# Performance work log

Hardware: AMD Instinct MI355X
Metric: run time of the kernel (lower is better)

Reference implementation:

```python
import jax, jax.numpy as jnp
import numpy as np
from jax import lax

B, D, H, W = 4, 32, 256, 256
ALPHA = 4.0     # init arg alpha
KFRAMES = 4.0   # self.K = alpha
EPS_BN = 1e-5

def FT2d(a):
    return jnp.fft.fft2(a, axes=(-2, -1))

def iFT2d(a):
    return jnp.fft.ifft2(a, axes=(-2, -1))

def forward_proj(field, otf):
    # field [B,D,H,W] real, otf [B,D,H,W] complex -> min-max scaled |holo| [B,1,H,W]
    Fholo = jnp.sum(FT2d(field.astype(jnp.complex64)) * otf, axis=1, keepdims=True)
    holo = jnp.abs(iFT2d(Fholo))
    mn = holo.min(axis=(-2, -1), keepdims=True)
    mx = holo.max(axis=(-2, -1), keepdims=True)
    return (holo - mn) / (mx - mn)

def back_proj(holo, otf):
    # holo [B,1,H,W] real -> real field [B,D,H,W]; broadcasting over depth == tile+FFT
    Fh = FT2d(holo.astype(jnp.complex64))
    return jnp.real(iFT2d(Fh * jnp.conj(otf)))

def cbl(xin, w, g, b, act):
    y = lax.conv_general_dilated(xin, w, (1, 1), 'SAME',
                                 dimension_numbers=('NCHW', 'OIHW', 'NCHW'))
    m = y.mean(axis=(0, 2, 3), keepdims=True)
    v = y.var(axis=(0, 2, 3), keepdims=True)  # biased var, torch BN training-mode
    y = (y - m) * lax.rsqrt(v + EPS_BN) * g[None, :, None, None] + b[None, :, None, None]
    return jax.nn.leaky_relu(y, 0.01) if act else y

def resblock(xin, wa, ga, ba, wb, gb, bb):
    h = cbl(cbl(xin, wa, ga, ba, True), wb, gb, bb, False)
    return jax.nn.leaky_relu(xin + h, 0.01)

def plholonet_forward(phi, z, u1, u2, otf, K1f, rho1, rho2, soft_thr, p):
    # ---- X update: FFT-domain proximal solve ----
    x1 = phi - u1
    x2 = z - u2
    n = rho1 * back_proj(x1, otf) + rho2 * x2
    d = (rho2 + jnp.abs(otf) ** 2 * rho1).astype(jnp.complex64)
    x = jnp.real(iFT2d(FT2d(n.astype(jnp.complex64)) / d))
    # ---- Phi update: vectorized 30-step masked bisection ----
    phi_tilde = forward_proj(x, otf) + u1
    K0 = 1.0 - K1f
    c = ALPHA / KFRAMES
    def func(y):
        return c * (K0 - K1f / (jnp.exp(c * y) - 1.0)) + rho1 * (y - phi_tilde)
    ind0_init = K1f == 0
    phimin = jnp.full_like(phi_tilde, 1e-5)
    phimax = jnp.full_like(phi_tilde, 100.0)
    phiave = 0.5 * (phimin + phimax)
    def step(carry, _):
        pmin, pmax, pave, ind0 = carry
        ind1 = jnp.logical_not(ind0)
        t = func(pave)
        pmin = jnp.where((t > 0) & ind1, pave, pmin)
        pmax = jnp.where((t < 0) & ind1, pave, pmax)
        ind0 = ind0 | ((t == 0) & ind1)
        pave = jnp.where(jnp.logical_not(ind0), 0.5 * (pmin + pmax), pave)
        return (pmin, pmax, pave, ind0), None
    (_, _, phiave, _), _ = lax.scan(step, (phimin, phimax, phiave, ind0_init), None, length=30)
    phi_next = jnp.where(ind0_init, phi_tilde - K0 / rho1, phiave)
    # ---- Z update: denoiser with symmetry loss ----
    z_tilde = x + u2
    h1 = resblock(z_tilde, p['w1a'], p['g1a'], p['b1a'], p['w1b'], p['g1b'], p['b1b'])
    h1_thr = jnp.sign(h1) * jax.nn.relu(jnp.abs(h1) - soft_thr)
    z_next = resblock(h1_thr, p['w2a'], p['g2a'], p['b2a'], p['w2b'], p['g2b'], p['b2b'])
    x_fb = resblock(h1, p['w2a'], p['g2a'], p['b2a'], p['w2b'], p['g2b'], p['b2b'])
    stage_symloss = x_fb - z_tilde
    # ---- dual updates ----
    u1_next = u1 + phi_next - forward_proj(x, otf)
    u2_next = u2 + z_next - x
    return (x, phi_next, z_next, u1_next, u2_next, stage_symloss)

def setup_inputs() -> dict:
    key = jax.random.key(0)
    ks = jax.random.split(key, 16)
    f = jnp.float32
    inp = dict(
        x=jax.random.normal(ks[0], (B, D, H, W), f),
        phi=jax.random.uniform(ks[1], (B, 1, H, W), dtype=f),
        z=jax.random.normal(ks[2], (B, D, H, W), f) * 0.1,
        u1=jax.random.uniform(ks[3], (B, 1, H, W), dtype=f) * 0.1,
        u2=jax.random.uniform(ks[4], (B, D, H, W), dtype=f) * 0.1,
        otf_real=jax.random.normal(ks[5], (B, D, H, W), f) * 0.5,
        otf_imag=jax.random.normal(ks[6], (B, D, H, W), f) * 0.5,
        K1=jax.random.randint(ks[7], (B, 1, H, W), 0, 5, jnp.int32),
        rho1=jnp.array([0.7], f),
        rho2=jnp.array([0.5], f),
        soft_thr=jnp.array([0.01], f),
    )
    for i, sfx in enumerate(['1a', '1b', '2a', '2b']):
        inp['w' + sfx] = jax.random.normal(ks[8 + i], (D, D, 3, 3), f) * 0.05
        inp['g' + sfx] = jnp.ones((D,), f)
        inp['b' + sfx] = jnp.zeros((D,), f)
    return inp

def reference(x, phi, z, u1, u2, otf_real, otf_imag, K1, rho1, rho2, soft_thr,
              w1a, g1a, b1a, w1b, g1b, b1b, w2a, g2a, b2a, w2b, g2b, b2b):
    # note: the torch forward immediately overwrites its `x` argument via X_update,
    # so the input x is unused (kept in the signature for interface faithfulness).
    otf = (otf_real + 1j * otf_imag).astype(jnp.complex64)
    K1f = K1.astype(jnp.float32)
    p = dict(w1a=w1a, g1a=g1a, b1a=b1a, w1b=w1b, g1b=g1b, b1b=b1b,
             w2a=w2a, g2a=g2a, b2a=b2a, w2b=w2b, g2b=g2b, b2b=b2b)
    return plholonet_forward(phi, z, u1, u2, otf, K1f, rho1, rho2, soft_thr, p)
```

## Files before the change

kernel.cpp:

```cpp
#include <hip/hip_runtime.h>
#include <math.h>

#define WDIM 256
#define HW   65536

struct cplx { float x, y; };
__device__ __forceinline__ cplx cmul(cplx a, cplx b){ return {a.x*b.x - a.y*b.y, a.x*b.y + a.y*b.x}; }
__device__ __forceinline__ cplx cadd(cplx a, cplx b){ return {a.x+b.x, a.y+b.y}; }
__device__ __forceinline__ cplx csub(cplx a, cplx b){ return {a.x-b.x, a.y-b.y}; }
__device__ __forceinline__ void swapc(cplx& a, cplx& b){ cplx t=a; a=b; b=t; }

typedef __attribute__((ext_vector_type(8))) short short8;
typedef __attribute__((ext_vector_type(4))) float float4v;

__device__ __forceinline__ unsigned short f2bf(float f){
  unsigned int u = __float_as_uint(f);
  unsigned int r = (u + 0x7FFFu + ((u >> 16) & 1u)) >> 16;
  return (unsigned short)r;
}
__device__ __forceinline__ float bf2f(unsigned short h){
  return __uint_as_float(((unsigned int)h) << 16);
}

template<bool INV>
__device__ __forceinline__ void fft16(cplx v[16]) {
  const float C16[8] = {1.f, 0.9238795325112867f, 0.7071067811865476f, 0.3826834323650898f,
                        0.f, -0.3826834323650898f, -0.7071067811865476f, -0.9238795325112867f};
  const float S16[8] = {0.f, 0.3826834323650898f, 0.7071067811865476f, 0.9238795325112867f,
                        1.f, 0.9238795325112867f, 0.7071067811865476f, 0.3826834323650898f};
  swapc(v[1], v[8]); swapc(v[2], v[4]); swapc(v[3], v[12]);
  swapc(v[5], v[10]); swapc(v[7], v[14]); swapc(v[11], v[13]);
  #pragma unroll
  for (int s = 1; s <= 4; ++s) {
    const int m = 1 << s, half = m >> 1, step = 16 >> s;
    #pragma unroll
    for (int k = 0; k < 16; k += m) {
      #pragma unroll
      for (int j = 0; j < half; ++j) {
        cplx w = {C16[j*step], INV ? S16[j*step] : -S16[j*step]};
        cplx t = cmul(w, v[k+j+half]);
        v[k+j+half] = csub(v[k+j], t);
        v[k+j]      = cadd(v[k+j], t);
      }
    }
  }
}

template<bool INV>
__device__ void fft256_16(cplx v[16], int t, cplx* Yu) {
  fft16<INV>(v);
  float ang = (INV ? 6.283185307179586f : -6.283185307179586f) * (float)t * (1.0f/256.0f);
  float sn, cs; sincosf(ang, &sn, &cs);
  cplx wstep = {cs, sn}, w = {1.f, 0.f};
  #pragma unroll
  for (int c = 0; c < 16; ++c) { v[c] = cmul(v[c], w); w = cmul(w, wstep); }
  __syncthreads();
  #pragma unroll
  for (int c = 0; c < 16; ++c) Yu[t*17 + c] = v[c];
  __syncthreads();
  cplx z[16];
  #pragma unroll
  for (int b = 0; b < 16; ++b) z[b] = Yu[b*17 + t];
  fft16<INV>(z);
  #pragma unroll
  for (int d = 0; d < 16; ++d) v[d] = z[d];
  __syncthreads();
}

__global__ __launch_bounds__(256) void k_row_fwd_all(const float* __restrict__ a,
                                                     const float* __restrict__ b,
                                                     const float* __restrict__ sa,
                                                     const float* __restrict__ sb,
                                                     cplx* __restrict__ P,
                                                     cplx* __restrict__ XS) {
  __shared__ cplx Y[16*280];
  int unit = threadIdx.x >> 4, t = threadIdx.x & 15;
  int bp = blockIdx.y;
  size_t rowoff = (size_t)(blockIdx.x*16 + unit)*WDIM;
  const float *pa, *pb;
  size_t base0, baseo_rel;
  cplx* outb;
  if (bp < 64) {
    int bb = bp >> 4, p = bp & 15;
    pa = a; pb = b;
    base0 = ((size_t)(bb*32 + 2*p))*HW + rowoff;
    outb = P; baseo_rel = (size_t)bp*HW + rowoff;
  } else {
    int pp = bp - 64;
    pa = sa; pb = sb;
    base0 = ((size_t)(2*pp))*HW + rowoff;
    outb = XS; baseo_rel = (size_t)pp*HW + rowoff;
  }
  size_t base1 = base0 + HW;
  cplx v[16];
  #pragma unroll
  for (int i = 0; i < 16; ++i) {
    size_t o = i*16 + t;
    v[i] = {pa[base0+o] - pb[base0+o], pa[base1+o] - pb[base1+o]};
  }
  fft256_16<false>(v, t, Y + unit*280);
  #pragma unroll
  for (int d = 0; d < 16; ++d) outb[baseo_rel + t + 16*d] = v[d];
}

template<bool INV>
__device__ void col_core(const cplx* __restrict__ in, cplx* lds, cplx v[16], size_t planeBase) {
  int tid = threadIdx.x;
  #pragma unroll
  for (int i = 0; i < 16; ++i) {
    int idx = tid + 256*i; int h = idx >> 4, w = idx & 15;
    lds[h*17 + w] = in[planeBase + (size_t)h*WDIM + w];
  }
  __syncthreads();
  int u = tid >> 4, t = tid & 15;
  cplx vv[16];
  #pragma unroll
  for (int a = 0; a < 16; ++a) vv[a] = lds[(16*a + t)*17 + u];
  fft256_16<INV>(vv, t, lds + u*280);
  #pragma unroll
  for (int d = 0; d < 16; ++d) v[d] = vv[d];
}

__global__ __launch_bounds__(256) void k_col_fwd_all(cplx* __restrict__ P,
                                                     cplx* __restrict__ XS) {
  __shared__ cplx lds[4480];
  int y = blockIdx.y;
  cplx* buf = (y < 64) ? (P + (size_t)y*HW) : (XS + (size_t)(y-64)*HW);
  size_t planeBase = blockIdx.x*16;
  cplx v[16];
  col_core<false>(buf, lds, v, planeBase);
  int u = threadIdx.x >> 4, t = threadIdx.x & 15;
  #pragma unroll
  for (int d = 0; d < 16; ++d) lds[(t + 16*d)*17 + u] = v[d];
  __syncthreads();
  int tid = threadIdx.x;
  #pragma unroll
  for (int i = 0; i < 16; ++i) {
    int idx = tid + 256*i; int h = idx >> 4, w = idx & 15;
    buf[planeBase + (size_t)h*WDIM + w] = lds[h*17 + w];
  }
}

__global__ __launch_bounds__(256) void k_row_inv_all(const cplx* __restrict__ Q,
                                                     const cplx* __restrict__ HFT,
                                                     cplx* __restrict__ W2,
                                                     cplx* __restrict__ XS) {
  __shared__ cplx Y[16*280];
  int unit = threadIdx.x >> 4, t = threadIdx.x & 15;
  int y = blockIdx.y;
  const cplx* inb;  cplx* outb;
  if (y < 64) { inb = Q + (size_t)y*HW; outb = W2 + (size_t)y*HW; }
  else        { inb = HFT + (size_t)(y-64)*HW; outb = XS + (size_t)(y-64)*HW; }
  size_t base = (size_t)(blockIdx.x*16 + unit)*WDIM;
  cplx v[16];
  #pragma unroll
  for (int i = 0; i < 16; ++i) v[i] = inb[base + i*16 + t];
  fft256_16<true>(v, t, Y + unit*280);
  #pragma unroll
  for (int d = 0; d < 16; ++d) outb[base + t + 16*d] = {v[d].x*(1.f/256.f), v[d].y*(1.f/256.f)};
}

__global__ __launch_bounds__(256) void k_col_inv_all(const cplx* __restrict__ W2,
                                                     const cplx* __restrict__ XS,
                                                     const float* __restrict__ u2,
                                                     float* __restrict__ xout,
                                                     unsigned short* __restrict__ ztcl,
                                                     float* __restrict__ holo,
                                                     float* __restrict__ partials) {
  __shared__ cplx lds[4480];
  int y = blockIdx.y;
  int tid = threadIdx.x;
  if (y < 64) {
    int bb = y >> 4, p = y & 15;
    cplx v[16];
    col_core<true>(W2 + (size_t)y*HW, lds, v, blockIdx.x*16);
    int u = tid >> 4, t = tid & 15;
    #pragma unroll
    for (int d = 0; d < 16; ++d) lds[(t + 16*d)*17 + u] = {v[d].x*(1.f/256.f), v[d].y*(1.f/256.f)};
    __syncthreads();
    size_t out0 = ((size_t)(bb*32 + 2*p))*HW + blockIdx.x*16;
    size_t out1 = out0 + HW;
    #pragma unroll
    for (int i = 0; i < 16; ++i) {
      int idx = tid + 256*i; int h = idx >> 4, w = idx & 15;
      cplx val = lds[h*17 + w];
      size_t g0 = out0 + (size_t)h*WDIM + w;
      size_t g1 = out1 + (size_t)h*WDIM + w;
      float zt0 = val.x + u2[g0];
      float zt1 = val.y + u2[g1];
      xout[g0] = val.x;
      xout[g1] = val.y;
      int pix = (h << 8) + (blockIdx.x << 4) + w;
      unsigned int pk = ((unsigned int)f2bf(zt1) << 16) | (unsigned int)f2bf(zt0);
      *(unsigned int*)(ztcl + ((((size_t)(bb << 16)) + pix) << 5) + 2*p) = pk;
    }
  } else {
    int py = y - 64;
    float* ldsf = (float*)lds;
    cplx v[16];
    col_core<true>(XS + (size_t)py*HW, lds, v, blockIdx.x*16);
    int u = tid >> 4, t = tid & 15;
    #pragma unroll
    for (int d = 0; d < 16; ++d) {
      float re = v[d].x*(1.f/256.f), im = v[d].y*(1.f/256.f);
      ldsf[(t + 16*d)*17 + u] = sqrtf(re*re + im*im);
    }
    __syncthreads();
    float mn = 1e30f, mx = -1e30f;
    size_t planeBase = (size_t)py*HW + blockIdx.x*16;
    #pragma unroll
    for (int i = 0; i < 16; ++i) {
      int idx = tid + 256*i; int h = idx >> 4, w = idx & 15;
      float val = ldsf[h*17 + w];
      holo[planeBase + (size_t)h*WDIM + w] = val;
      mn = fminf(mn, val); mx = fmaxf(mx, val);
    }
    __syncthreads();
    #pragma unroll
    for (int s = 1; s < 64; s <<= 1) { mn = fminf(mn, __shfl_xor(mn, s)); mx = fmaxf(mx, __shfl_xor(mx, s)); }
    if ((tid & 63) == 0) { ldsf[(tid>>6)*2] = mn; ldsf[(tid>>6)*2 + 1] = mx; }
    __syncthreads();
    if (tid == 0) {
      float a = fminf(fminf(ldsf[0], ldsf[2]), fminf(ldsf[4], ldsf[6]));
      float b = fmaxf(fmaxf(ldsf[1], ldsf[3]), fmaxf(ldsf[5], ldsf[7]));
      partials[(py*16 + blockIdx.x)*2]     = a;
      partials[(py*16 + blockIdx.x)*2 + 1] = b;
    }
  }
}

__global__ __launch_bounds__(64) void k_mm_reduce(const float* __restrict__ partials,
                                                  float* __restrict__ minmax) {
  int t = threadIdx.x; int b = t >> 4, i = t & 15;
  float mn = partials[(b*16 + i)*2], mx = partials[(b*16 + i)*2 + 1];
  #pragma unroll
  for (int s = 1; s < 16; s <<= 1) { mn = fminf(mn, __shfl_xor(mn, s)); mx = fmaxf(mx, __shfl_xor(mx, s)); }
  if (i == 0) { minmax[b*2] = mn; minmax[b*2 + 1] = mx; }
}

__global__ __launch_bounds__(256) void k_combine_hf(const cplx* __restrict__ P,
                                                    cplx* __restrict__ Q,
                                                    const cplx* __restrict__ XS,
                                                    const float* __restrict__ otr,
                                                    const float* __restrict__ oti,
                                                    const float* __restrict__ r1p,
                                                    const float* __restrict__ r2p,
                                                    cplx* __restrict__ HF) {
  int j = blockIdx.x*256 + threadIdx.x;
  int b = j / 33024;
  int r = j - b*33024;
  int kh = r >> 8, kw = r & 255;
  if ((kh == 0 || kh == 128) && kw > 128) return;
  int k  = (kh << 8) | kw;
  int k2 = ((((256 - kh) & 255)) << 8) | ((256 - kw) & 255);
  float rho1 = r1p[0], rho2 = r2p[0];
  int c = b >> 1, par = b & 1;
  cplx Sk = XS[(c << 16) | k], Sm = XS[(c << 16) | k2];
  cplx A;
  if (par == 0) A = {0.5f*(Sk.x + Sm.x), 0.5f*(Sk.y - Sm.y)};
  else          A = {0.5f*(Sk.y + Sm.y), 0.5f*(Sm.x - Sk.x)};
  cplx Am = {A.x, -A.y};
  float hfr = 0.f, hfi = 0.f, hfr2 = 0.f, hfi2 = 0.f;
  #pragma unroll 1
  for (int p = 0; p < 16; ++p) {
    int pb = (b*16 + p) << 16;
    cplx Pk = P[pb | k], Pm = P[pb | k2];
    float Zr[2], Zi[2];
    Zr[0] = 0.5f*(Pk.x + Pm.x); Zi[0] = 0.5f*(Pk.y - Pm.y);
    Zr[1] = 0.5f*(Pk.y + Pm.y); Zi[1] = 0.5f*(Pm.x - Pk.x);
    float Xr[2], Xi[2];
    #pragma unroll
    for (int dd = 0; dd < 2; ++dd) {
      int db = (b*32 + 2*p + dd) << 16;
      float or1 = otr[db | k],  oi1 = oti[db | k];
      float or2 = otr[db | k2], oi2 = oti[db | k2];
      float Gr = 0.5f*(A.x*or1 + A.y*oi1 + Am.x*or2 + Am.y*oi2);
      float Gi = 0.5f*(A.y*or1 - A.x*oi1 + Am.x*oi2 - Am.y*or2);
      float di = 0.5f*(1.f/(rho2 + rho1*(or1*or1 + oi1*oi1))
                     + 1.f/(rho2 + rho1*(or2*or2 + oi2*oi2)));
      float xr = (rho1*Gr + rho2*Zr[dd])*di;
      float xi = (rho1*Gi + rho2*Zi[dd])*di;
      Xr[dd] = xr; Xi[dd] = xi;
      hfr  += xr*or1 - xi*oi1;
      hfi  += xr*oi1 + xi*or1;
      hfr2 += xr*or2 + xi*oi2;
      hfi2 += xr*oi2 - xi*or2;
    }
    Q[pb | k]  = {Xr[0] - Xi[1], Xi[0] + Xr[1]};
    Q[pb | k2] = {Xr[0] + Xi[1], Xr[1] - Xi[0]};
  }
  HF[(b << 16) | k]  = {hfr,  hfi};
  HF[(b << 16) | k2] = {hfr2, hfi2};
}

__global__ __launch_bounds__(256) void k_bisect(const float* __restrict__ holo,
                                                const float* __restrict__ minmax,
                                                const float* __restrict__ u1,
                                                const int* __restrict__ K1,
                                                const float* __restrict__ r1p,
                                                float* __restrict__ phi_out,
                                                float* __restrict__ u1_out) {
  int i = blockIdx.x*256 + threadIdx.x;
  int b = i >> 16;
  float mn = minmax[2*b], mx = minmax[2*b + 1];
  float fp = (holo[i] - mn) / (mx - mn);
  float pt = fp + u1[i];
  float K1f = (float)K1[i];
  float K0 = 1.f - K1f;
  float rho1 = r1p[0];
  bool ind0i = (K1f == 0.f);
  bool ind0 = ind0i;
  float pmin = 1e-5f, pmax = 100.f, pave = 0.5f*(pmin + pmax);
  #pragma unroll 1
  for (int it = 0; it < 30; ++it) {
    float e = expf(pave);
    float t = (K0 - K1f/(e - 1.f)) + rho1*(pave - pt);
    bool ind1 = !ind0;
    if (t > 0.f && ind1) pmin = pave;
    if (t < 0.f && ind1) pmax = pave;
    ind0 = ind0 || (t == 0.f && ind1);
    if (!ind0) pave = 0.5f*(pmin + pmax);
  }
  float pn = ind0i ? (pt - K0/rho1) : pave;
  phi_out[i] = pn;
  u1_out[i]  = u1[i] + pn - fp;
}

__global__ __launch_bounds__(256) void k_wprep(const float* __restrict__ w1a,
                                               const float* __restrict__ w1b,
                                               const float* __restrict__ w2a,
                                               const float* __restrict__ w2b,
                                               unsigned short* __restrict__ Ap) {
  int idx = blockIdx.x*256 + threadIdx.x;
  if (idx >= 4*9216) return;
  int wsel = idx / 9216, r = idx - wsel*9216;
  const float* w = wsel==0 ? w1a : wsel==1 ? w1b : wsel==2 ? w2a : w2b;
  int tap = r / 1024, r2 = r - tap*1024, oc = r2 >> 5, ic = r2 & 31;
  Ap[idx] = f2bf(w[(oc*32 + ic)*9 + tap]);
}

#define CONV_R 4
__global__ __launch_bounds__(256, 4) void k_conv(const unsigned short* __restrict__ inCL,
                                                 const unsigned short* __restrict__ Aprep,
                                                 unsigned short* __restrict__ outCL,
                                                 float* __restrict__ part,
                                                 int mode,
                                                 const float* __restrict__ scsh,
                                                 const float* __restrict__ thrp) {
  __shared__ unsigned short tile[6*66*32];
  __shared__ float sred[4][16][2];
  int tid = threadIdx.x;
  int bx = blockIdx.x, by = blockIdx.y, bz = blockIdx.z;
  int w0 = bx*64, h0 = by*CONV_R;

  for (int idx = tid; idx < 6*264; idx += 256) {
    int lrow = idx/264, rem = idx - lrow*264;
    int lcol = rem >> 2, m = rem & 3;
    int grow = h0 - 1 + lrow, gcol = w0 - 1 + lcol;
    uint4 val = {0,0,0,0};
    if (grow >= 0 && grow < 256 && gcol >= 0 && gcol < 256) {
      uint4 raw = *(const uint4*)(inCL + (((size_t)(bz<<16) + (grow<<8) + gcol)<<5) + m*8);
      if (mode == 0) val = raw;
      else {
        unsigned short h8[8]; *(uint4*)h8 = raw;
        #pragma unroll
        for (int j = 0; j < 8; ++j) {
          float v = bf2f(h8[j]);
          int ic = m*8+j; v = v*scsh[ic] + scsh[32+ic]; v = v > 0.f ? v : 0.01f*v;
          h8[j] = f2bf(v);
        }
        val = *(uint4*)h8;
      }
    }
    *(uint4*)&tile[(size_t)idx*8] = val;
  }

  int lane = tid & 63, w = tid >> 6;
  int q = lane >> 4, ln = lane & 15;
  int ocH = w & 1, s0 = w >> 1;
  short8 afrag[9];
  #pragma unroll
  for (int t = 0; t < 9; ++t)
    afrag[t] = *(const short8*)(Aprep + ((t*32 + ocH*16 + ln)*32 + q*8));
  __syncthreads();

  float sacc[4] = {0,0,0,0}, s2acc[4] = {0,0,0,0};
  #pragma unroll
  for (int r = 0; r < CONV_R; ++r) {
    #pragma unroll
    for (int si = 0; si < 2; ++si) {
      int s = s0 + si*2;
      float4v acc = {0.f, 0.f, 0.f, 0.f};
      #pragma unroll
      for (int t = 0; t < 9; ++t) {
        int dy = t/3, dx = t - dy*3;
        int lrow = r + dy, lcol = s*16 + ln + dx;
        const short8 bfrag = *(const short8*)&tile[(lrow*66 + lcol)*32 + q*8];
        acc = __builtin_amdgcn_mfma_f32_16x16x32_bf16(afrag[t], bfrag, acc, 0, 0, 0);
      }
      int px = w0 + s*16 + ln, row = h0 + r;
      size_t obase = ((((size_t)(bz<<16) + (row<<8) + px))<<5) + ocH*16 + q*4;
      unsigned short o4[4];
      #pragma unroll
      for (int u = 0; u < 4; ++u) { o4[u] = f2bf(acc[u]); sacc[u] += acc[u]; s2acc[u] += acc[u]*acc[u]; }
      *(uint2*)(outCL + obase) = *(uint2*)o4;
    }
  }

  #pragma unroll
  for (int u = 0; u < 4; ++u) {
    float a = sacc[u], b2 = s2acc[u];
    #pragma unroll
    for (int mq = 1; mq < 16; mq <<= 1) { a += __shfl_xor(a, mq); b2 += __shfl_xor(b2, mq); }
    if (ln == 0) { sred[w][q*4+u][0] = a; sred[w][q*4+u][1] = b2; }
  }
  __syncthreads();
  if (tid < 64) {
    int ocH2 = tid >> 5, i16 = (tid >> 1) & 15, st = tid & 1;
    float tot = sred[ocH2][i16][st] + sred[ocH2+2][i16][st];
    int oc = ocH2*16 + i16;
    int blk = ((bz<<6) + by)*4 + bx;
    part[(oc*2+st)*1024 + blk] = tot;
  }
}

__global__ __launch_bounds__(256, 3) void k_conv35(const unsigned short* __restrict__ inCL,
                                                   const unsigned short* __restrict__ Aprep,
                                                   unsigned short* __restrict__ outT,
                                                   unsigned short* __restrict__ outR,
                                                   float* __restrict__ partT,
                                                   float* __restrict__ partR,
                                                   const float* __restrict__ thrp) {
  __shared__ unsigned short tileR[6*66*32];
  __shared__ unsigned short tileT[6*66*32];
  __shared__ float sredT[4][16][2];
  __shared__ float sredR[4][16][2];
  int tid = threadIdx.x;
  int bx = blockIdx.x, by = blockIdx.y, bz = blockIdx.z;
  int w0 = bx*64, h0 = by*CONV_R;
  float thr = thrp[0];

  for (int idx = tid; idx < 6*264; idx += 256) {
    int lrow = idx/264, rem = idx - lrow*264;
    int lcol = rem >> 2, m = rem & 3;
    int grow = h0 - 1 + lrow, gcol = w0 - 1 + lcol;
    uint4 raw = {0,0,0,0}, thrv = {0,0,0,0};
    if (grow >= 0 && grow < 256 && gcol >= 0 && gcol < 256) {
      raw = *(const uint4*)(inCL + (((size_t)(bz<<16) + (grow<<8) + gcol)<<5) + m*8);
      unsigned short h8[8], t8[8]; *(uint4*)h8 = raw;
      #pragma unroll
      for (int j = 0; j < 8; ++j) {
        float v = bf2f(h8[j]);
        float s = fabsf(v) - thr; s = s > 0.f ? s : 0.f;
        t8[j] = f2bf(copysignf(s, v));
      }
      thrv = *(uint4*)t8;
    }
    *(uint4*)&tileR[(size_t)idx*8] = raw;
    *(uint4*)&tileT[(size_t)idx*8] = thrv;
  }

  int lane = tid & 63, w = tid >> 6;
  int q = lane >> 4, ln = lane & 15;
  int ocH = w & 1, s0 = w >> 1;
  short8 afrag[9];
  #pragma unroll
  for (int t = 0; t < 9; ++t)
    afrag[t] = *(const short8*)(Aprep + ((t*32 + ocH*16 + ln)*32 + q*8));
  __syncthreads();

  float saT[4] = {0,0,0,0}, s2T[4] = {0,0,0,0};
  float saR[4] = {0,0,0,0}, s2R[4] = {0,0,0,0};
  #pragma unroll
  for (int r = 0; r < CONV_R; ++r) {
    #pragma unroll
    for (int si = 0; si < 2; ++si) {
      int s = s0 + si*2;
      float4v accT = {0.f,0.f,0.f,0.f}, accR = {0.f,0.f,0.f,0.f};
      #pragma unroll
      for (int t = 0; t < 9; ++t) {
        int dy = t/3, dx = t - dy*3;
        int lrow = r + dy, lcol = s*16 + ln + dx;
        size_t off = ((size_t)(lrow*66 + lcol))*32 + q*8;
        const short8 bT = *(const short8*)&tileT[off];
        accT = __builtin_amdgcn_mfma_f32_16x16x32_bf16(afrag[t], bT, accT, 0, 0, 0);
        const short8 bR = *(const short8*)&tileR[off];
        accR = __builtin_amdgcn_mfma_f32_16x16x32_bf16(afrag[t], bR, accR, 0, 0, 0);
      }
      int px = w0 + s*16 + ln, row = h0 + r;
      size_t obase = ((((size_t)(bz<<16) + (row<<8) + px))<<5) + ocH*16 + q*4;
      unsigned short oT[4], oR[4];
      #pragma unroll
      for (int u = 0; u < 4; ++u) {
        oT[u] = f2bf(accT[u]); saT[u] += accT[u]; s2T[u] += accT[u]*accT[u];
        oR[u] = f2bf(accR[u]); saR[u] += accR[u]; s2R[u] += accR[u]*accR[u];
      }
      *(uint2*)(outT + obase) = *(uint2*)oT;
      *(uint2*)(outR + obase) = *(uint2*)oR;
    }
  }

  #pragma unroll
  for (int u = 0; u < 4; ++u) {
    float aT = saT[u], bT2 = s2T[u], aR = saR[u], bR2 = s2R[u];
    #pragma unroll
    for (int mq = 1; mq < 16; mq <<= 1) {
      aT += __shfl_xor(aT, mq); bT2 += __shfl_xor(bT2, mq);
      aR += __shfl_xor(aR, mq); bR2 += __shfl_xor(bR2, mq);
    }
    if (ln == 0) {
      sredT[w][q*4+u][0] = aT; sredT[w][q*4+u][1] = bT2;
      sredR[w][q*4+u][0] = aR; sredR[w][q*4+u][1] = bR2;
    }
  }
  __syncthreads();
  if (tid < 64) {
    int ocH2 = tid >> 5, i16 = (tid >> 1) & 15, st = tid & 1;
    int oc = ocH2*16 + i16;
    int blk = ((bz<<6) + by)*4 + bx;
    partT[(oc*2+st)*1024 + blk] = sredT[ocH2][i16][st] + sredT[ocH2+2][i16][st];
    partR[(oc*2+st)*1024 + blk] = sredR[ocH2][i16][st] + sredR[ocH2+2][i16][st];
  }
}

__global__ __launch_bounds__(256, 4) void k_conv_pair(const unsigned short* __restrict__ inA,
                                                      const unsigned short* __restrict__ inB,
                                                      unsigned short* __restrict__ outA,
                                                      unsigned short* __restrict__ outB,
                                                      float* __restrict__ partA,
                                                      float* __restrict__ partB,
                                                      const float* __restrict__ ssA,
                                                      const float* __restrict__ ssB,
                                                      const unsigned short* __restrict__ Aprep) {
  __shared__ unsigned short tile[6*66*32];
  __shared__ float sred[4][16][2];
  int tid = threadIdx.x;
  int bx = blockIdx.x, by = blockIdx.y;
  int half = blockIdx.z >> 2, bz = blockIdx.z & 3;
  const unsigned short* inCL = half ? inB : inA;
  unsigned short* outCL = half ? outB : outA;
  const float* scsh = half ? ssB : ssA;
  float* part = half ? partB : partA;
  int w0 = bx*64, h0 = by*CONV_R;

  for (int idx = tid; idx < 6*264; idx += 256) {
    int lrow = idx/264, rem = idx - lrow*264;
    int lcol = rem >> 2, m = rem & 3;
    int grow = h0 - 1 + lrow, gcol = w0 - 1 + lcol;
    uint4 val = {0,0,0,0};
    if (grow >= 0 && grow < 256 && gcol >= 0 && gcol < 256) {
      uint4 raw = *(const uint4*)(inCL + (((size_t)(bz<<16) + (grow<<8) + gcol)<<5) + m*8);
      unsigned short h8[8]; *(uint4*)h8 = raw;
      #pragma unroll
      for (int j = 0; j < 8; ++j) {
        float v = bf2f(h8[j]);
        int ic = m*8+j; v = v*scsh[ic] + scsh[32+ic]; v = v > 0.f ? v : 0.01f*v;
        h8[j] = f2bf(v);
      }
      val = *(uint4*)h8;
    }
    *(uint4*)&tile[(size_t)idx*8] = val;
  }

  int lane = tid & 63, w = tid >> 6;
  int q = lane >> 4, ln = lane & 15;
  int ocH = w & 1, s0 = w >> 1;
  short8 afrag[9];
  #pragma unroll
  for (int t = 0; t < 9; ++t)
    afrag[t] = *(const short8*)(Aprep + ((t*32 + ocH*16 + ln)*32 + q*8));
  __syncthreads();

  float sacc[4] = {0,0,0,0}, s2acc[4] = {0,0,0,0};
  #pragma unroll
  for (int r = 0; r < CONV_R; ++r) {
    #pragma unroll
    for (int si = 0; si < 2; ++si) {
      int s = s0 + si*2;
      float4v acc = {0.f, 0.f, 0.f, 0.f};
      #pragma unroll
      for (int t = 0; t < 9; ++t) {
        int dy = t/3, dx = t - dy*3;
        int lrow = r + dy, lcol = s*16 + ln + dx;
        const short8 bfrag = *(const short8*)&tile[(lrow*66 + lcol)*32 + q*8];
        acc = __builtin_amdgcn_mfma_f32_16x16x32_bf16(afrag[t], bfrag, acc, 0, 0, 0);
      }
      int px = w0 + s*16 + ln, row = h0 + r;
      size_t obase = ((((size_t)(bz<<16) + (row<<8) + px))<<5) + ocH*16 + q*4;
      unsigned short o4[4];
      #pragma unroll
      for (int u = 0; u < 4; ++u) { o4[u] = f2bf(acc[u]); sacc[u] += acc[u]; s2acc[u] += acc[u]*acc[u]; }
      *(uint2*)(outCL + obase) = *(uint2*)o4;
    }
  }

  #pragma unroll
  for (int u = 0; u < 4; ++u) {
    float a = sacc[u], b2 = s2acc[u];
    #pragma unroll
    for (int mq = 1; mq < 16; mq <<= 1) { a += __shfl_xor(a, mq); b2 += __shfl_xor(b2, mq); }
    if (ln == 0) { sred[w][q*4+u][0] = a; sred[w][q*4+u][1] = b2; }
  }
  __syncthreads();
  if (tid < 64) {
    int ocH2 = tid >> 5, i16 = (tid >> 1) & 15, st = tid & 1;
    float tot = sred[ocH2][i16][st] + sred[ocH2+2][i16][st];
    int oc = ocH2*16 + i16;
    int blk = ((bz<<6) + by)*4 + bx;
    part[(oc*2+st)*1024 + blk] = tot;
  }
}

__global__ __launch_bounds__(256) void k_finstats2(const float* __restrict__ part,
                                                   const float* __restrict__ g,
                                                   const float* __restrict__ beta,
                                                   float* __restrict__ SS) {
  __shared__ float red[8];
  int oc = blockIdx.x, t = threadIdx.x;
  const float* ps = part + oc*2048;
  float s  = ps[t] + ps[t+256] + ps[t+512] + ps[t+768];
  float s2 = ps[1024+t] + ps[1280+t] + ps[1536+t] + ps[1792+t];
  #pragma unroll
  for (int m = 1; m < 64; m <<= 1) { s += __shfl_xor(s, m); s2 += __shfl_xor(s2, m); }
  if ((t & 63) == 0) { red[(t>>6)*2] = s; red[(t>>6)*2+1] = s2; }
  __syncthreads();
  if (t == 0) {
    float S  = red[0] + red[2] + red[4] + red[6];
    float S2 = red[1] + red[3] + red[5] + red[7];
    const float N = 262144.f;
    float mean = S / N;
    float var  = S2 / N - mean*mean;
    float sc = g[oc] * rsqrtf(var + 1e-5f);
    SS[oc] = sc; SS[32+oc] = beta[oc] - mean*sc;
  }
}

__global__ __launch_bounds__(256) void k_finstats_dual(const float* __restrict__ pA,
                                                       const float* __restrict__ pB,
                                                       const float* __restrict__ g,
                                                       const float* __restrict__ beta,
                                                       float* __restrict__ SSa,
                                                       float* __restrict__ SSc) {
  __shared__ float red[8];
  int bxi = blockIdx.x;
  const float* part = bxi < 32 ? pA : pB;
  float* SS = bxi < 32 ? SSa : SSc;
  int oc = bxi & 31, t = threadIdx.x;
  const float* ps = part + oc*2048;
  float s  = ps[t] + ps[t+256] + ps[t+512] + ps[t+768];
  float s2 = ps[1024+t] + ps[1280+t] + ps[1536+t] + ps[1792+t];
  #pragma unroll
  for (int m = 1; m < 64; m <<= 1) { s += __shfl_xor(s, m); s2 += __shfl_xor(s2, m); }
  if ((t & 63) == 0) { red[(t>>6)*2] = s; red[(t>>6)*2+1] = s2; }
  __syncthreads();
  if (t == 0) {
    float S  = red[0] + red[2] + red[4] + red[6];
    float S2 = red[1] + red[3] + red[5] + red[7];
    const float N = 262144.f;
    float mean = S / N;
    float var  = S2 / N - mean*mean;
    float sc = g[oc] * rsqrtf(var + 1e-5f);
    SS[oc] = sc; SS[32+oc] = beta[oc] - mean*sc;
  }
}

__global__ __launch_bounds__(256) void k_h1cl(const unsigned short* __restrict__ zt,
                                              const unsigned short* __restrict__ c2,
                                              const float* __restrict__ SS,
                                              unsigned short* __restrict__ h1) {
  int idx = blockIdx.x*256 + threadIdx.x;
  int cg = idx & 3;
  uint4 za = *(const uint4*)(zt + (size_t)idx*8);
  uint4 ca = *(const uint4*)(c2 + (size_t)idx*8);
  unsigned short zs[8], cs[8], os[8];
  *(uint4*)zs = za; *(uint4*)cs = ca;
  #pragma unroll
  for (int j = 0; j < 8; ++j) {
    int c = cg*8 + j;
    float v = bf2f(zs[j]) + bf2f(cs[j])*SS[c] + SS[32+c];
    v = v > 0.f ? v : 0.01f*v;
    os[j] = f2bf(v);
  }
  *(uint4*)(h1 + (size_t)idx*8) = *(uint4*)os;
}

__global__ __launch_bounds__(256) void k_finalAB(const unsigned short* __restrict__ h1,
                                                 const unsigned short* __restrict__ c4,
                                                 const unsigned short* __restrict__ c6,
                                                 const unsigned short* __restrict__ ztcl,
                                                 const float* __restrict__ SS4,
                                                 const float* __restrict__ SS6,
                                                 const float* __restrict__ thrp,
                                                 const float* __restrict__ u2,
                                                 const float* __restrict__ x,
                                                 float* __restrict__ zout,
                                                 float* __restrict__ u2out,
                                                 float* __restrict__ symout) {
  __shared__ float zT[32*66];
  __shared__ float sT[32*66];
  int tid = threadIdx.x;
  size_t b = blockIdx.y;
  int px0 = blockIdx.x*64;
  float thr = thrp[0];
  int px = tid >> 2, cg = tid & 3;
  size_t cbase = ((((b<<16) + px0 + px))<<5) + cg*8;
  uint4 ha = *(const uint4*)(h1 + cbase);
  uint4 c4a = *(const uint4*)(c4 + cbase);
  uint4 c6a = *(const uint4*)(c6 + cbase);
  uint4 za = *(const uint4*)(ztcl + cbase);
  unsigned short hs[8], c4s[8], c6s[8], zs[8];
  *(uint4*)hs = ha; *(uint4*)c4s = c4a; *(uint4*)c6s = c6a; *(uint4*)zs = za;
  #pragma unroll
  for (int j = 0; j < 8; ++j) {
    int c = cg*8+j;
    float hv = bf2f(hs[j]);
    float s = fabsf(hv) - thr; s = s > 0.f ? s : 0.f;
    float th = copysignf(s, hv);
    float zv = th + bf2f(c4s[j])*SS4[c] + SS4[32+c];
    zT[c*66 + px] = zv > 0.f ? zv : 0.01f*zv;
    float xv = hv + bf2f(c6s[j])*SS6[c] + SS6[32+c];
    xv = xv > 0.f ? xv : 0.01f*xv;
    sT[c*66 + px] = xv - bf2f(zs[j]);
  }
  __syncthreads();
  #pragma unroll
  for (int i = 0; i < 2; ++i) {
    int ch = tid + i*256; int c = ch >> 4, p4 = (ch & 15)*4;
    size_t g = ((b*32 + c)<<16) + px0 + p4;
    float4 uv = *(const float4*)(u2 + g);
    float4 xv = *(const float4*)(x + g);
    float4 zv = { zT[c*66+p4], zT[c*66+p4+1], zT[c*66+p4+2], zT[c*66+p4+3] };
    float4 un = { uv.x+zv.x-xv.x, uv.y+zv.y-xv.y, uv.z+zv.z-xv.z, uv.w+zv.w-xv.w };
    float4 sv = { sT[c*66+p4], sT[c*66+p4+1], sT[c*66+p4+2], sT[c*66+p4+3] };
    *(float4*)(zout + g) = zv;
    *(float4*)(u2out + g) = un;
    *(float4*)(symout + g) = sv;
  }
}

extern "C" void kernel_launch(void* const* d_in, const int* in_sizes, int n_in,
                              void* d_out, int out_size, void* d_ws, size_t ws_size,
                              hipStream_t stream) {
  const float* phi  = (const float*)d_in[1];
  const float* z    = (const float*)d_in[2];
  const float* u1   = (const float*)d_in[3];
  const float* u2   = (const float*)d_in[4];
  const float* otr  = (const float*)d_in[5];
  const float* oti  = (const float*)d_in[6];
  const int*   K1   = (const int*)d_in[7];
  const float* rho1 = (const float*)d_in[8];
  const float* rho2 = (const float*)d_in[9];
  const float* sthr = (const float*)d_in[10];
  const float* w1a = (const float*)d_in[11];
  const float* g1a = (const float*)d_in[12];
  const float* b1a = (const float*)d_in[13];
  const float* w1b = (const float*)d_in[14];
  const float* g1b = (const float*)d_in[15];
  const float* b1b = (const float*)d_in[16];
  const float* w2a = (const float*)d_in[17];
  const float* g2a = (const float*)d_in[18];
  const float* b2a = (const float*)d_in[19];
  const float* w2b = (const float*)d_in[20];
  const float* g2b = (const float*)d_in[21];
  const float* b2b = (const float*)d_in[22];

  float* out = (float*)d_out;
  float* x_out   = out;
  float* phi_out = out + 8388608;
  float* z_out   = out + 8650752;
  float* u1_out  = out + 17039360;
  float* u2_out  = out + 17301504;
  float* sym_out = out + 25690112;

  char* ws = (char*)d_ws;
  cplx*  P     = (cplx*)ws;
  cplx*  Q     = (cplx*)(ws + 33554432);
  cplx*  XS    = (cplx*)(ws + 67108864);
  cplx*  HFT   = (cplx*)(ws + 69206016);
  float* holo  = (float*)(ws + 71303168);
  float* partmm= (float*)(ws + 72351744);
  float* mm    = (float*)(ws + 72355840);

  unsigned short* Ap    = (unsigned short*)(ws + 71303168);
  float*          part  = (float*)(ws + 71434240);
  float*          partB = (float*)(ws + 69206016);
  float*          SSb   = (float*)(ws + 71696384);
  unsigned short* ZTcl  = (unsigned short*)(ws + 33554432);
  unsigned short* H1cl  = (unsigned short*)(ws + 50331648);
  unsigned short* C4cl  = (unsigned short*)(ws + 0);
  unsigned short* C2cl  = (unsigned short*)(ws + 16777216);
  unsigned short* C6cl  = (unsigned short*)(ws + 16777216);
  unsigned short* C135a = (unsigned short*)z_out;
  unsigned short* C135b = (unsigned short*)((char*)z_out + 16777216);
  cplx* W2 = (cplx*)z_out;

  k_row_fwd_all <<<dim3(16, 66), 256, 0, stream>>>(z, u2, phi, u1, P, XS);
  k_col_fwd_all <<<dim3(16, 66), 256, 0, stream>>>(P, XS);
  k_combine_hf  <<<516, 256, 0, stream>>>(P, Q, XS, otr, oti, rho1, rho2, HFT);
  k_row_inv_all <<<dim3(16, 68), 256, 0, stream>>>(Q, HFT, W2, XS);
  k_col_inv_all <<<dim3(16, 68), 256, 0, stream>>>(W2, XS, u2, x_out, ZTcl, holo, partmm);
  k_mm_reduce   <<<1, 64, 0, stream>>>(partmm, mm);
  k_bisect<<<1024, 256, 0, stream>>>(holo, mm, u1, K1, rho1, phi_out, u1_out);

  k_wprep<<<144, 256, 0, stream>>>(w1a, w1b, w2a, w2b, Ap);

  dim3 cg(4, 64, 4);
  k_conv<<<cg, 256, 0, stream>>>(ZTcl, Ap + 0,      C135a, part, 0, SSb,     sthr);
  k_finstats2<<<32, 256, 0, stream>>>(part, g1a, b1a, SSb + 0);
  k_conv<<<cg, 256, 0, stream>>>(C135a, Ap + 9216,  C2cl,  part, 1, SSb + 0, sthr);
  k_finstats2<<<32, 256, 0, stream>>>(part, g1b, b1b, SSb + 64);
  k_h1cl<<<4096, 256, 0, stream>>>(ZTcl, C2cl, SSb + 64, H1cl);

  k_conv35<<<cg, 256, 0, stream>>>(H1cl, Ap + 18432, C135a, C135b, part, partB, sthr);
  k_finstats_dual<<<64, 256, 0, stream>>>(part, partB, g2a, b2a, SSb + 128, SSb + 256);
  k_conv_pair<<<dim3(4, 64, 8), 256, 0, stream>>>(C135a, C135b, C4cl, C6cl,
                                                  part, partB, SSb + 128, SSb + 256,
                                                  Ap + 27648);
  k_finstats_dual<<<64, 256, 0, stream>>>(part, partB, g2b, b2b, SSb + 192, SSb + 320);

  k_finalAB<<<dim3(1024, 4), 256, 0, stream>>>(H1cl, C4cl, C6cl, ZTcl,
                                               SSb + 192, SSb + 320, sthr, u2, x_out,
                                               z_out, u2_out, sym_out);
}
```

Before: 501.1 us.

## Fuse spectral combine with inverse row FFT and fold small kernels into neighbors

Merges the frequency-domain combine step with the inverse row FFT, so each block computes the combined spectra for a row pair straight into shared memory and transforms them there, avoiding a full write and re-read of the Q and HF intermediates. The min/max reduction moves into the bisection kernel and the weight-prep work is folded into an extra slice of the forward row-FFT grid, which removes three launches. The fused kernel uses only 516 blocks with serial per-plane loops and extra barriers, so it may expose less parallelism and latency hiding than the separate kernels did.

Result: faster. 482.7 us (-3.7%).

```diff
diff --git a/kernel.cpp b/kernel.cpp
--- a/kernel.cpp
+++ b/kernel.cpp
@@ -72,10 +72,26 @@
                                                      const float* __restrict__ sa,
                                                      const float* __restrict__ sb,
                                                      cplx* __restrict__ P,
-                                                     cplx* __restrict__ XS) {
+                                                     cplx* __restrict__ XS,
+                                                     const float* __restrict__ w1a,
+                                                     const float* __restrict__ w1b,
+                                                     const float* __restrict__ w2a,
+                                                     const float* __restrict__ w2b,
+                                                     unsigned short* __restrict__ Ap) {
   __shared__ cplx Y[16*280];
+  int bp = blockIdx.y;
+  if (bp == 66) {
+    int base = blockIdx.x * 2304;
+    for (int r = threadIdx.x; r < 2304; r += 256) {
+      int idx = base + r;
+      int wsel = idx / 9216, rr = idx - wsel*9216;
+      const float* w = wsel==0 ? w1a : wsel==1 ? w1b : wsel==2 ? w2a : w2b;
+      int tap = rr / 1024, r2 = rr - tap*1024, oc = r2 >> 5, ic = r2 & 31;
+      Ap[idx] = f2bf(w[(oc*32 + ic)*9 + tap]);
+    }
+    return;
+  }
   int unit = threadIdx.x >> 4, t = threadIdx.x & 15;
-  int bp = blockIdx.y;
   size_t rowoff = (size_t)(blockIdx.x*16 + unit)*WDIM;
   const float *pa, *pb;
   size_t base0, baseo_rel;
@@ -141,23 +157,95 @@
   }
 }
 
-__global__ __launch_bounds__(256) void k_row_inv_all(const cplx* __restrict__ Q,
-                                                     const cplx* __restrict__ HFT,
+__global__ __launch_bounds__(256) void k_combine_inv(const cplx* __restrict__ P,
+                                                     const cplx* __restrict__ XS,
+                                                     const float* __restrict__ otr,
+                                                     const float* __restrict__ oti,
+                                                     const float* __restrict__ r1p,
+                                                     const float* __restrict__ r2p,
                                                      cplx* __restrict__ W2,
-                                                     cplx* __restrict__ XS) {
-  __shared__ cplx Y[16*280];
+                                                     cplx* __restrict__ HFX) {
+  __shared__ cplx R[16*273];
+  int kw = threadIdx.x;
+  int kh = blockIdx.x;
+  int b  = blockIdx.y;
+  int kh2 = (256 - kh) & 255;
+  int kw2 = (256 - kw) & 255;
+  int k  = (kh << 8) | kw;
+  int k2 = (kh2 << 8) | kw2;
+  float rho1 = r1p[0], rho2 = r2p[0];
+  int c = b >> 1, par = b & 1;
+  cplx Sk = XS[(c << 16) | k], Sm = XS[(c << 16) | k2];
+  cplx A;
+  if (par == 0) A = {0.5f*(Sk.x + Sm.x), 0.5f*(Sk.y - Sm.y)};
+  else          A = {0.5f*(Sk.y + Sm.y), 0.5f*(Sm.x - Sk.x)};
+  cplx Am = {A.x, -A.y};
+  float hfr = 0.f, hfi = 0.f, hfr2 = 0.f, hfi2 = 0.f;
   int unit = threadIdx.x >> 4, t = threadIdx.x & 15;
-  int y = blockIdx.y;
-  const cplx* inb;  cplx* outb;
-  if (y < 64) { inb = Q + (size_t)y*HW; outb = W2 + (size_t)y*HW; }
-  else        { inb = HFT + (size_t)(y-64)*HW; outb = XS + (size_t)(y-64)*HW; }
-  size_t base = (size_t)(blockIdx.x*16 + unit)*WDIM;
-  cplx v[16];
-  #pragma unroll
-  for (int i = 0; i < 16; ++i) v[i] = inb[base + i*16 + t];
-  fft256_16<true>(v, t, Y + unit*280);
-  #pragma unroll
-  for (int d = 0; d < 16; ++d) outb[base + t + 16*d] = {v[d].x*(1.f/256.f), v[d].y*(1.f/256.f)};
+
+  #pragma unroll 1
+  for (int half = 0; half < 2; ++half) {
+    #pragma unroll 1
+    for (int pl = 0; pl < 8; ++pl) {
+      int p = half*8 + pl;
+      int pb = (b*16 + p) << 16;
+      cplx Pk = P[pb | k], Pm = P[pb | k2];
+      float Zr[2], Zi[2];
+      Zr[0] = 0.5f*(Pk.x + Pm.x); Zi[0] = 0.5f*(Pk.y - Pm.y);
+      Zr[1] = 0.5f*(Pk.y + Pm.y); Zi[1] = 0.5f*(Pm.x - Pk.x);
+      float Xr[2], Xi[2];
+      #pragma unroll
+      for (int dd = 0; dd < 2; ++dd) {
+        int db = (b*32 + 2*p + dd) << 16;
+        float or1 = otr[db | k],  oi1 = oti[db | k];
+        float or2 = otr[db | k2], oi2 = oti[db | k2];
+        float Gr = 0.5f*(A.x*or1 + A.y*oi1 + Am.x*or2 + Am.y*oi2);
+        float Gi = 0.5f*(A.y*or1 - A.x*oi1 + Am.x*oi2 - Am.y*or2);
+        float di = 0.5f*(1.f/(rho2 + rho1*(or1*or1 + oi1*oi1))
+                       + 1.f/(rho2 + rho1*(or2*or2 + oi2*oi2)));
+        float xr = (rho1*Gr + rho2*Zr[dd])*di;
+        float xi = (rho1*Gi + rho2*Zi[dd])*di;
+        Xr[dd] = xr; Xi[dd] = xi;
+        hfr  += xr*or1 - xi*oi1;
+        hfi  += xr*oi1 + xi*or1;
+        hfr2 += xr*or2 + xi*oi2;
+        hfi2 += xr*oi2 - xi*or2;
+      }
+      R[(pl*2)*273 + kw]    = {Xr[0] - Xi[1], Xi[0] + Xr[1]};
+      R[(pl*2+1)*273 + kw2] = {Xr[0] + Xi[1], Xr[1] - Xi[0]};
+    }
+    __syncthreads();
+    {
+      cplx* slot = R + unit*273;
+      cplx v[16];
+      #pragma unroll
+      for (int i = 0; i < 16; ++i) v[i] = slot[i*16 + t];
+      fft256_16<true>(v, t, slot);
+      int plane = b*16 + half*8 + (unit >> 1);
+      int row = (unit & 1) ? kh2 : kh;
+      size_t base = (size_t)plane*HW + (size_t)row*WDIM;
+      #pragma unroll
+      for (int d = 0; d < 16; ++d)
+        W2[base + t + 16*d] = {v[d].x*(1.f/256.f), v[d].y*(1.f/256.f)};
+    }
+  }
+  R[0*273 + kw]  = {hfr,  hfi};
+  R[1*273 + kw2] = {hfr2, hfi2};
+  __syncthreads();
+  {
+    cplx* slot = R + (unit & 1)*273;
+    cplx v[16];
+    #pragma unroll
+    for (int i = 0; i < 16; ++i) v[i] = slot[i*16 + t];
+    fft256_16<true>(v, t, slot);
+    if (unit < 2) {
+      int row = unit ? kh2 : kh;
+      size_t base = (size_t)b*HW + (size_t)row*WDIM;
+      #pragma unroll
+      for (int d = 0; d < 16; ++d)
+        HFX[base + t + 16*d] = {v[d].x*(1.f/256.f), v[d].y*(1.f/256.f)};
+    }
+  }
 }
 
 __global__ __launch_bounds__(256) void k_col_inv_all(const cplx* __restrict__ W2,
@@ -229,80 +317,25 @@
   }
 }
 
-__global__ __launch_bounds__(64) void k_mm_reduce(const float* __restrict__ partials,
-                                                  float* __restrict__ minmax) {
-  int t = threadIdx.x; int b = t >> 4, i = t & 15;
-  float mn = partials[(b*16 + i)*2], mx = partials[(b*16 + i)*2 + 1];
-  #pragma unroll
-  for (int s = 1; s < 16; s <<= 1) { mn = fminf(mn, __shfl_xor(mn, s)); mx = fmaxf(mx, __shfl_xor(mx, s)); }
-  if (i == 0) { minmax[b*2] = mn; minmax[b*2 + 1] = mx; }
-}
-
-__global__ __launch_bounds__(256) void k_combine_hf(const cplx* __restrict__ P,
-                                                    cplx* __restrict__ Q,
-                                                    const cplx* __restrict__ XS,
-                                                    const float* __restrict__ otr,
-                                                    const float* __restrict__ oti,
-                                                    const float* __restrict__ r1p,
-                                                    const float* __restrict__ r2p,
-                                                    cplx* __restrict__ HF) {
-  int j = blockIdx.x*256 + threadIdx.x;
-  int b = j / 33024;
-  int r = j - b*33024;
-  int kh = r >> 8, kw = r & 255;
-  if ((kh == 0 || kh == 128) && kw > 128) return;
-  int k  = (kh << 8) | kw;
-  int k2 = ((((256 - kh) & 255)) << 8) | ((256 - kw) & 255);
-  float rho1 = r1p[0], rho2 = r2p[0];
-  int c = b >> 1, par = b & 1;
-  cplx Sk = XS[(c << 16) | k], Sm = XS[(c << 16) | k2];
-  cplx A;
-  if (par == 0) A = {0.5f*(Sk.x + Sm.x), 0.5f*(Sk.y - Sm.y)};
-  else          A = {0.5f*(Sk.y + Sm.y), 0.5f*(Sm.x - Sk.x)};
-  cplx Am = {A.x, -A.y};
-  float hfr = 0.f, hfi = 0.f, hfr2 = 0.f, hfi2 = 0.f;
-  #pragma unroll 1
-  for (int p = 0; p < 16; ++p) {
-    int pb = (b*16 + p) << 16;
-    cplx Pk = P[pb | k], Pm = P[pb | k2];
-    float Zr[2], Zi[2];
-    Zr[0] = 0.5f*(Pk.x + Pm.x); Zi[0] = 0.5f*(Pk.y - Pm.y);
-    Zr[1] = 0.5f*(Pk.y + Pm.y); Zi[1] = 0.5f*(Pm.x - Pk.x);
-    float Xr[2], Xi[2];
-    #pragma unroll
-    for (int dd = 0; dd < 2; ++dd) {
-      int db = (b*32 + 2*p + dd) << 16;
-      float or1 = otr[db | k],  oi1 = oti[db | k];
-      float or2 = otr[db | k2], oi2 = oti[db | k2];
-      float Gr = 0.5f*(A.x*or1 + A.y*oi1 + Am.x*or2 + Am.y*oi2);
-      float Gi = 0.5f*(A.y*or1 - A.x*oi1 + Am.x*oi2 - Am.y*or2);
-      float di = 0.5f*(1.f/(rho2 + rho1*(or1*or1 + oi1*oi1))
-                     + 1.f/(rho2 + rho1*(or2*or2 + oi2*oi2)));
-      float xr = (rho1*Gr + rho2*Zr[dd])*di;
-      float xi = (rho1*Gi + rho2*Zi[dd])*di;
-      Xr[dd] = xr; Xi[dd] = xi;
-      hfr  += xr*or1 - xi*oi1;
-      hfi  += xr*oi1 + xi*or1;
-      hfr2 += xr*or2 + xi*oi2;
-      hfi2 += xr*oi2 - xi*or2;
-    }
-    Q[pb | k]  = {Xr[0] - Xi[1], Xi[0] + Xr[1]};
-    Q[pb | k2] = {Xr[0] + Xi[1], Xr[1] - Xi[0]};
-  }
-  HF[(b << 16) | k]  = {hfr,  hfi};
-  HF[(b << 16) | k2] = {hfr2, hfi2};
-}
-
 __global__ __launch_bounds__(256) void k_bisect(const float* __restrict__ holo,
-                                                const float* __restrict__ minmax,
+                                                const float* __restrict__ partials,
                                                 const float* __restrict__ u1,
                                                 const int* __restrict__ K1,
                                                 const float* __restrict__ r1p,
                                                 float* __restrict__ phi_out,
                                                 float* __restrict__ u1_out) {
+  __shared__ float red2[2];
   int i = blockIdx.x*256 + threadIdx.x;
   int b = i >> 16;
-  float mn = minmax[2*b], mx = minmax[2*b + 1];
+  if (threadIdx.x < 16) {
+    float mn = partials[(b*16 + threadIdx.x)*2];
+    float mx = partials[(b*16 + threadIdx.x)*2 + 1];
+    #pragma unroll
+    for (int s = 1; s < 16; s <<= 1) { mn = fminf(mn, __shfl_xor(mn, s)); mx = fmaxf(mx, __shfl_xor(mx, s)); }
+    if (threadIdx.x == 0) { red2[0] = mn; red2[1] = mx; }
+  }
+  __syncthreads();
+  float mn = red2[0], mx = red2[1];
   float fp = (holo[i] - mn) / (mx - mn);
   float pt = fp + u1[i];
   float K1f = (float)K1[i];
@@ -324,19 +357,6 @@
   float pn = ind0i ? (pt - K0/rho1) : pave;
   phi_out[i] = pn;
   u1_out[i]  = u1[i] + pn - fp;
-}
-
-__global__ __launch_bounds__(256) void k_wprep(const float* __restrict__ w1a,
-                                               const float* __restrict__ w1b,
-                                               const float* __restrict__ w2a,
-                                               const float* __restrict__ w2b,
-                                               unsigned short* __restrict__ Ap) {
-  int idx = blockIdx.x*256 + threadIdx.x;
-  if (idx >= 4*9216) return;
-  int wsel = idx / 9216, r = idx - wsel*9216;
-  const float* w = wsel==0 ? w1a : wsel==1 ? w1b : wsel==2 ? w2a : w2b;
-  int tap = r / 1024, r2 = r - tap*1024, oc = r2 >> 5, ic = r2 & 31;
-  Ap[idx] = f2bf(w[(oc*32 + ic)*9 + tap]);
 }
 
 #define CONV_R 4
@@ -774,14 +794,12 @@
 
   char* ws = (char*)d_ws;
   cplx*  P     = (cplx*)ws;
-  cplx*  Q     = (cplx*)(ws + 33554432);
   cplx*  XS    = (cplx*)(ws + 67108864);
-  cplx*  HFT   = (cplx*)(ws + 69206016);
+  cplx*  HFX   = (cplx*)(ws + 69206016);
   float* holo  = (float*)(ws + 71303168);
   float* partmm= (float*)(ws + 72351744);
-  float* mm    = (float*)(ws + 72355840);
-
-  unsigned short* Ap    = (unsigned short*)(ws + 71303168);
+
+  unsigned short* Ap    = (unsigned short*)(ws + 68157440);
   float*          part  = (float*)(ws + 71434240);
   float*          partB = (float*)(ws + 69206016);
   float*          SSb   = (float*)(ws + 71696384);
@@ -794,15 +812,12 @@
   unsigned short* C135b = (unsigned short*)((char*)z_out + 16777216);
   cplx* W2 = (cplx*)z_out;
 
-  k_row_fwd_all <<<dim3(16, 66), 256, 0, stream>>>(z, u2, phi, u1, P, XS);
+  k_row_fwd_all <<<dim3(16, 67), 256, 0, stream>>>(z, u2, phi, u1, P, XS,
+                                                   w1a, w1b, w2a, w2b, Ap);
   k_col_fwd_all <<<dim3(16, 66), 256, 0, stream>>>(P, XS);
-  k_combine_hf  <<<516, 256, 0, stream>>>(P, Q, XS, otr, oti, rho1, rho2, HFT);
-  k_row_inv_all <<<dim3(16, 68), 256, 0, stream>>>(Q, HFT, W2, XS);
-  k_col_inv_all <<<dim3(16, 68), 256, 0, stream>>>(W2, XS, u2, x_out, ZTcl, holo, partmm);
-  k_mm_reduce   <<<1, 64, 0, stream>>>(partmm, mm);
-  k_bisect<<<1024, 256, 0, stream>>>(holo, mm, u1, K1, rho1, phi_out, u1_out);
-
-  k_wprep<<<144, 256, 0, stream>>>(w1a, w1b, w2a, w2b, Ap);
+  k_combine_inv <<<dim3(129, 4), 256, 0, stream>>>(P, XS, otr, oti, rho1, rho2, W2, HFX);
+  k_col_inv_all <<<dim3(16, 68), 256, 0, stream>>>(W2, HFX, u2, x_out, ZTcl, holo, partmm);
+  k_bisect<<<1024, 256, 0, stream>>>(holo, partmm, u1, K1, rho1, phi_out, u1_out);
 
   dim3 cg(4, 64, 4);
   k_conv<<<cg, 256, 0, stream>>>(ZTcl, Ap + 0,      C135a, part, 0, SSb,     sthr);
```
